# Performance work log

Measured on AMD Instinct MI355X. Metric: run time of the kernel, lower is better.

## Reference

```python
import jax
import jax.numpy as jnp
import numpy as np

ALPHA = 0.95
NUM_POS_FREQS = 4
CROSS_WEIGHT = 0.5
TOPK = 16
EPS = 1e-12


def _pos_enc(coords):
    # coords: [N, 4] -> [N, 4 * 2 * NUM_POS_FREQS]
    N = coords.shape[0]
    freqs = 2.0 ** jnp.arange(NUM_POS_FREQS, dtype=coords.dtype)  # [F]
    angles = coords[:, :, None] * (2.0 * jnp.pi) * freqs          # [N,4,F]
    pe = jnp.concatenate([jnp.sin(angles), jnp.cos(angles)], axis=-1)  # [N,4,2F]
    return pe.reshape(N, -1)


def _cosine_sim(x, y):
    # row-wise cosine similarity: [N,C] x [M,C] -> [N,M]
    xn = x / jnp.maximum(jnp.linalg.norm(x, axis=-1, keepdims=True), EPS)
    yn = y / jnp.maximum(jnp.linalg.norm(y, axis=-1, keepdims=True), EPS)
    return xn @ yn.T


def _sparsify_topk(A, k):
    # row-wise top-k, self-loop always kept (diag forced to max before top-k)
    N = A.shape[0]
    diag = jnp.arange(N)
    A_with_self = A.at[diag, diag].set(jnp.finfo(A.dtype).max)
    _, topk_idx = jax.lax.top_k(A_with_self, k)                   # [N,k]
    mask = jnp.zeros(A.shape, dtype=bool).at[diag[:, None], topk_idx].set(True)
    return jnp.where(mask, A, jnp.zeros((), A.dtype))


def _sym_normalize(A):
    deg = jnp.clip(A.sum(axis=-1, keepdims=True), EPS, None)      # [N,1]
    d_inv_sqrt = deg ** -0.5
    return d_inv_sqrt * A * d_inv_sqrt.T


def _build_adjacency(features, coordinates, history_features, history_coords):
    B, C = features.shape
    n, K, _ = history_features.shape
    H = n * K

    cur_feats = features
    cur_pos = _pos_enc(coordinates)
    A_cur = ALPHA * _cosine_sim(cur_feats, cur_feats) + (1.0 - ALPHA) * _cosine_sim(cur_pos, cur_pos)

    hist_feats = history_features.reshape(H, C)
    hist_pos = _pos_enc(history_coords.reshape(H, 4))
    A_hist = ALPHA * _cosine_sim(hist_feats, hist_feats) + (1.0 - ALPHA) * _cosine_sim(hist_pos, hist_pos)

    A_cross = ALPHA * _cosine_sim(cur_feats, hist_feats) + (1.0 - ALPHA) * _cosine_sim(cur_pos, hist_pos)
    A_cross = CROSS_WEIGHT * A_cross

    A = jnp.block([[A_cur, A_cross], [A_cross.T, A_hist]])        # [N,N], N=B+H
    node_feats = jnp.concatenate([cur_feats, hist_feats], axis=0)

    N = A.shape[0]
    if TOPK is not None and TOPK < N:
        A = _sparsify_topk(A, TOPK)
    A = _sym_normalize(A)
    return A[None], node_feats[None]


def setup_inputs() -> dict:
    key = jax.random.key(0)
    k1, k2, k3, k4 = jax.random.split(key, 4)
    B, C, n, K = 4096, 256, 128, 32
    return {
        "features": jax.random.normal(k1, (B, C), dtype=jnp.float32),
        "coordinates": jax.random.uniform(k2, (B, 4), dtype=jnp.float32),
        "history_features": jax.random.normal(k3, (n, K, C), dtype=jnp.float32),
        "history_coords": jax.random.uniform(k4, (n, K, 4), dtype=jnp.float32),
    }


def reference(features, coordinates, history_features, history_coords):
    adj, node_feats = _build_adjacency(features, coordinates, history_features, history_coords)
    return adj, node_feats
```

## Files before the change

kernel.cpp:

```cpp
#include <hip/hip_runtime.h>
#include <math.h>

#define B_CUR 4096
#define N_TOT 8192
#define C_F   256
#define C_TOT 288
#define KSEL  16
#define NTILE 64

typedef unsigned short u16;
typedef __attribute__((ext_vector_type(8))) short short8;
typedef __attribute__((ext_vector_type(4))) float floatx4;

__device__ inline float bf2f(u16 v) {
  union { unsigned int u; float f; } x; x.u = ((unsigned int)v) << 16; return x.f;
}
__device__ inline u16 f2bf(float f) {
  union { float f; unsigned int u; } x; x.f = f;
  unsigned int u = x.u;
  u += ((u >> 16) & 1u) + 0x7FFFu;
  return (u16)(u >> 16);
}

#define GLD_LDS16(g, l) __builtin_amdgcn_global_load_lds(                      \
    (const __attribute__((address_space(1))) unsigned int*)(g),                \
    (__attribute__((address_space(3))) unsigned int*)(l), 16, 0, 0)

__global__ __launch_bounds__(256) void k_prep(
    const float* __restrict__ feats, const float* __restrict__ hfeats,
    const float* __restrict__ coords, const float* __restrict__ hcoords,
    u16* __restrict__ Zb, float* __restrict__ out_nf) {
  int wave = threadIdx.x >> 6;
  int lane = threadIdx.x & 63;
  int row  = blockIdx.x * 4 + wave;
  const float* src = (row < B_CUR) ? (feats + (size_t)row * C_F)
                                   : (hfeats + (size_t)(row - B_CUR) * C_F);
  int c0 = lane * 4;
  float4 raw = *(const float4*)(src + c0);
  float ss = raw.x*raw.x + raw.y*raw.y + raw.z*raw.z + raw.w*raw.w;
  #pragma unroll
  for (int m = 32; m; m >>= 1) ss += __shfl_xor(ss, m, 64);
  float scale = 0.97467943448089633f / fmaxf(sqrtf(ss), 1e-12f);
  ushort4 o;
  o.x = f2bf(raw.x*scale); o.y = f2bf(raw.y*scale);
  o.z = f2bf(raw.z*scale); o.w = f2bf(raw.w*scale);
  *(ushort4*)(Zb + (size_t)row * C_TOT + c0) = o;
  *(float4*)(out_nf + (size_t)row * C_F + c0) = raw;

  const float* csrc = (row < B_CUR) ? (coords + (size_t)row * 4)
                                    : (hcoords + (size_t)(row - B_CUR) * 4);
  int d = lane >> 3, sc = (lane >> 2) & 1, f = lane & 3;
  float c = csrc[d & 3];
  float ang = c * 6.283185307179586f * (float)(1 << f);
  float pe = sc ? cosf(ang) : sinf(ang);
  float p2 = pe * pe;
  #pragma unroll
  for (int m = 16; m; m >>= 1) p2 += __shfl_xor(p2, m, 64);
  float pscale = 0.22360679774997896f / fmaxf(sqrtf(p2), 1e-12f);
  if (lane < 32) Zb[(size_t)row * C_TOT + C_F + lane] = f2bf(pe * pscale);
}

#define EP_STRIDE 136
__global__ __launch_bounds__(256) void k_gemm_mfma(const u16* __restrict__ Zb,
                                                   u16* __restrict__ adj16) {
  __shared__ __align__(16) u16 smem[2 * 128 * 96];
  u16* As = smem;
  u16* Bs = smem + 128 * 96;
  int tid  = threadIdx.x;

  int t = blockIdx.x;
  int bi = (int)floorf(((2.0f*NTILE + 1.0f) -
            sqrtf((float)((2*NTILE+1)*(2*NTILE+1)) - 8.0f*(float)t)) * 0.5f);
  if (bi < 0) bi = 0; if (bi > NTILE-1) bi = NTILE-1;
  while (bi > 0 && t < bi*NTILE - bi*(bi-1)/2) --bi;
  while (bi < NTILE-1 && t >= (bi+1)*NTILE - (bi+1)*bi/2) ++bi;
  int bj = bi + (t - (bi*NTILE - bi*(bi-1)/2));

  int wave = tid >> 6, lane = tid & 63;
  int quad = lane >> 4, l16 = lane & 15;
  int m0w  = (wave >> 1) * 64;
  int n0w  = (wave & 1) * 64;
  int i0   = bi * 128, j0 = bj * 128;

  floatx4 acc[4][4];
  #pragma unroll
  for (int a = 0; a < 4; ++a)
    #pragma unroll
    for (int b = 0; b < 4; ++b) acc[a][b] = (floatx4){0.f, 0.f, 0.f, 0.f};

  for (int kt = 0; kt < C_TOT; kt += 96) {
    #pragma unroll
    for (int it = 0; it < 6; ++it) {
      int s   = it * 256 + tid;
      int row = s / 12, seg = s % 12;
      const u16* ga = Zb + (size_t)(i0 + row) * C_TOT + kt + seg * 8;
      const u16* gb = Zb + (size_t)(j0 + row) * C_TOT + kt + seg * 8;
      GLD_LDS16(ga, As + s * 8);
      GLD_LDS16(gb, Bs + s * 8);
    }
    __builtin_amdgcn_s_waitcnt(0);
    __syncthreads();
    #pragma unroll
    for (int ks = 0; ks < 3; ++ks) {
      short8 af[4], bf[4];
      #pragma unroll
      for (int mi = 0; mi < 4; ++mi)
        af[mi] = *(const short8*)(&As[(m0w + mi*16 + l16) * 96 + ks*32 + quad*8]);
      #pragma unroll
      for (int ni = 0; ni < 4; ++ni)
        bf[ni] = *(const short8*)(&Bs[(n0w + ni*16 + l16) * 96 + ks*32 + quad*8]);
      #pragma unroll
      for (int mi = 0; mi < 4; ++mi)
        #pragma unroll
        for (int ni = 0; ni < 4; ++ni)
          acc[mi][ni] = __builtin_amdgcn_mfma_f32_16x16x32_bf16(
              af[mi], bf[ni], acc[mi][ni], 0, 0, 0);
    }
    __syncthreads();
  }

  float w = ((bi < 32) != (bj < 32)) ? 0.5f : 1.0f;

  #pragma unroll
  for (int mi = 0; mi < 4; ++mi) {
    #pragma unroll
    for (int ni = 0; ni < 4; ++ni) {
      int col = n0w + ni * 16 + l16;
      #pragma unroll
      for (int rg = 0; rg < 4; ++rg) {
        int row = m0w + mi * 16 + quad * 4 + rg;
        smem[row * EP_STRIDE + col] = f2bf(acc[mi][ni][rg] * w);
      }
    }
  }
  __syncthreads();
  #pragma unroll
  for (int it = 0; it < 8; ++it) {
    int idx = it * 256 + tid;
    int row = idx >> 4, l = idx & 15;
    uint4 v = *(const uint4*)(&smem[row * EP_STRIDE + l * 8]);
    *(uint4*)(&adj16[(size_t)(i0 + row) * 16384 + j0 + l * 8]) = v;
  }

  if (bi != bj) {
    __syncthreads();
    #pragma unroll
    for (int mi = 0; mi < 4; ++mi) {
      #pragma unroll
      for (int ni = 0; ni < 4; ++ni) {
        int col = n0w + ni * 16 + l16;
        #pragma unroll
        for (int rg = 0; rg < 4; ++rg) {
          int row = m0w + mi * 16 + quad * 4 + rg;
          smem[col * EP_STRIDE + row] = f2bf(acc[mi][ni][rg] * w);
        }
      }
    }
    __syncthreads();
    #pragma unroll
    for (int it = 0; it < 8; ++it) {
      int idx = it * 256 + tid;
      int row = idx >> 4, l = idx & 15;
      uint4 v = *(const uint4*)(&smem[row * EP_STRIDE + l * 8]);
      *(uint4*)(&adj16[(size_t)(j0 + row) * 16384 + i0 + l * 8]) = v;
    }
  }
}

__global__ __launch_bounds__(256) void k_topk(
    const u16* adj16, float* adj,
    int* __restrict__ topk_idx, float* __restrict__ topk_val,
    float* __restrict__ deg_out) {
  __shared__ unsigned int cand[64];
  __shared__ float s_diag;
  int r = blockIdx.x;
  int t = threadIdx.x;
  int wave = t >> 6, lane = t & 63;
  const u16* rowp = adj16 + (size_t)r * 16384;

  uint4 raw[4];
  #pragma unroll
  for (int j = 0; j < 4; ++j)
    raw[j] = *(const uint4*)(rowp + j * 2048 + t * 8);
  if (t == 0) s_diag = bf2f(rowp[r]);
  __syncthreads();

  {
    float* oro = adj + (size_t)r * N_TOT;
    const float4 z4 = make_float4(0.f, 0.f, 0.f, 0.f);
    #pragma unroll
    for (int kk = 0; kk < 8; ++kk)
      *(float4*)(oro + kk * 1024 + t * 4) = z4;
  }

  unsigned int keys[32];
  #pragma unroll
  for (int j = 0; j < 4; ++j) {
    int c0 = j * 2048 + t * 8;
    u16 e[8]; *(uint4*)e = raw[j];
    #pragma unroll
    for (int q = 0; q < 8; ++q) {
      int col = c0 + q;
      unsigned int b = e[q];
      unsigned int s16 = (b & 0x8000u) ? (b ^ 0xFFFFu) : (b | 0x8000u);
      unsigned int k = (s16 << 16) | (unsigned int)(8191 - col);
      if (col == r) k = 0xFFFF0000u | (unsigned int)(8191 - r);
      keys[j * 8 + q] = k;
    }
  }

  unsigned int m1 = 0, m2 = 0; int i1 = 0, i2 = 0;
  #pragma unroll
  for (int i = 0; i < 32; ++i) {
    unsigned int k = keys[i];
    if (k > m1) { m2 = m1; i2 = i1; m1 = k; i1 = i; }
    else if (k > m2) { m2 = k; i2 = i; }
  }
  unsigned int taken = 0;

  for (int it = 0; it < KSEL; ++it) {
    unsigned int wmax = m1;
    #pragma unroll
    for (int s = 32; s; s >>= 1) {
      unsigned int o = (unsigned int)__shfl_xor((int)wmax, s, 64);
      wmax = (o > wmax) ? o : wmax;
    }
    if (lane == it) cand[wave * 16 + it] = wmax;
    if (m1 == wmax && m1 != 0) {
      taken |= 1u << i1;
      if (m2 != 0) { m1 = m2; i1 = i2; m2 = 0; }
      else {
        m1 = 0; m2 = 0; i1 = 0; i2 = 0;
        #pragma unroll
        for (int i = 0; i < 32; ++i) {
          unsigned int k = (taken & (1u << i)) ? 0u : keys[i];
          if (k > m1) { m2 = m1; i2 = i1; m1 = k; i1 = i; }
          else if (k > m2) { m2 = k; i2 = i; }
        }
      }
    }
  }
  __syncthreads();

  if (wave == 0) {
    unsigned int c = cand[lane];
    unsigned int myWin = 0;
    for (int it = 0; it < KSEL; ++it) {
      unsigned int wmax = c;
      #pragma unroll
      for (int s = 32; s; s >>= 1) {
        unsigned int o = (unsigned int)__shfl_xor((int)wmax, s, 64);
        wmax = (o > wmax) ? o : wmax;
      }
      if (c == wmax) c = 0;
      if (lane == it) myWin = wmax;
    }
    float val = 0.f;
    int col = 0;
    if (lane < KSEL) {
      unsigned int p = myWin;
      col = 8191 - (int)(p & 0x1FFFu);
      unsigned int k16 = p >> 16;
      unsigned int b = (k16 & 0x8000u) ? (k16 ^ 0x8000u) : ((~k16) & 0xFFFFu);
      val = (col == r) ? s_diag : bf2f((u16)b);
      topk_idx[r * KSEL + lane] = col;
      topk_val[r * KSEL + lane] = val;
    }
    float s = (lane < KSEL) ? val : 0.f;
    #pragma unroll
    for (int m = 8; m; m >>= 1) s += __shfl_xor(s, m, 64);
    if (lane == 0) deg_out[r] = s;
  }
}

__global__ void k_scale(float* __restrict__ adj, const int* __restrict__ topk_idx,
                        const float* __restrict__ topk_val,
                        const float* __restrict__ deg) {
  int g = blockIdx.x * blockDim.x + threadIdx.x;
  if (g >= N_TOT * KSEL) return;
  int r = g >> 4, m = g & 15;
  int j = topk_idx[r * KSEL + m];
  if (j < 0) j = 0; if (j >= N_TOT) j = N_TOT - 1;
  float v = topk_val[r * KSEL + m];
  float di = 1.0f / sqrtf(fmaxf(deg[r], 1e-12f));
  float dj = 1.0f / sqrtf(fmaxf(deg[j], 1e-12f));
  adj[(size_t)r * N_TOT + j] = v * di * dj;
}

extern "C" void kernel_launch(void* const* d_in, const int* in_sizes, int n_in,
                              void* d_out, int out_size, void* d_ws, size_t ws_size,
                              hipStream_t stream) {
  const float* feats   = (const float*)d_in[0];
  const float* coords  = (const float*)d_in[1];
  const float* hfeats  = (const float*)d_in[2];
  const float* hcoords = (const float*)d_in[3];
  float* out    = (float*)d_out;
  float* adj    = out;
  u16*   adj16  = (u16*)out;
  float* out_nf = out + (size_t)N_TOT * N_TOT;

  char* ws    = (char*)d_ws;
  u16*  Zb    = (u16*)ws;
  size_t zb   = (size_t)N_TOT * C_TOT * sizeof(u16);
  zb = (zb + 255) & ~(size_t)255;
  int*   t_idx = (int*)(ws + zb);
  float* t_val = (float*)(ws + zb + (size_t)N_TOT*KSEL*sizeof(int));
  float* deg   = (float*)(ws + zb + (size_t)N_TOT*KSEL*(sizeof(int)+sizeof(float)));

  hipLaunchKernelGGL(k_prep, dim3(N_TOT/4), dim3(256), 0, stream,
                     feats, hfeats, coords, hcoords, Zb, out_nf);
  hipLaunchKernelGGL(k_gemm_mfma, dim3(NTILE*(NTILE+1)/2), dim3(256), 0, stream,
                     Zb, adj16);
  hipLaunchKernelGGL(k_topk, dim3(N_TOT), dim3(256), 0, stream,
                     adj16, adj, t_idx, t_val, deg);
  hipLaunchKernelGGL(k_scale, dim3((N_TOT*KSEL + 255)/256), dim3(256), 0, stream,
                     adj, t_idx, t_val, deg);
}
```

Baseline: 386.7 us.

## Double-buffer GEMM K-loop, move bf16 scores to workspace, nontemporal zero stores

The GEMM K-loop now uses 32-wide K slices with double-buffered LDS, so the next slice's global-to-LDS loads overlap the MFMAs on the current one. The bf16 score matrix moves out of the output buffer, where it was stored with a 16384 stride, into a separate workspace region with a compact 8192 stride. That lets k_topk drop a barrier and zero its output rows with nontemporal stores without clobbering unread scores. The cost is more loop iterations and barriers in the GEMM, plus extra workspace memory.

```diff
diff --git a/kernel.cpp b/kernel.cpp
--- a/kernel.cpp
+++ b/kernel.cpp
@@ -62,10 +62,8 @@
 
 #define EP_STRIDE 136
 __global__ __launch_bounds__(256) void k_gemm_mfma(const u16* __restrict__ Zb,
-                                                   u16* __restrict__ adj16) {
-  __shared__ __align__(16) u16 smem[2 * 128 * 96];
-  u16* As = smem;
-  u16* Bs = smem + 128 * 96;
+                                                   u16* __restrict__ s16) {
+  __shared__ __align__(16) u16 smem[17408];
   int tid  = threadIdx.x;
 
   int t = blockIdx.x;
@@ -82,40 +80,59 @@
   int n0w  = (wave & 1) * 64;
   int i0   = bi * 128, j0 = bj * 128;
 
+  int srow0 = tid >> 2;
+  int scol0 = (tid & 3) * 8;
+
   floatx4 acc[4][4];
   #pragma unroll
   for (int a = 0; a < 4; ++a)
     #pragma unroll
     for (int b = 0; b < 4; ++b) acc[a][b] = (floatx4){0.f, 0.f, 0.f, 0.f};
 
-  for (int kt = 0; kt < C_TOT; kt += 96) {
-    #pragma unroll
-    for (int it = 0; it < 6; ++it) {
-      int s   = it * 256 + tid;
-      int row = s / 12, seg = s % 12;
-      const u16* ga = Zb + (size_t)(i0 + row) * C_TOT + kt + seg * 8;
-      const u16* gb = Zb + (size_t)(j0 + row) * C_TOT + kt + seg * 8;
-      GLD_LDS16(ga, As + s * 8);
-      GLD_LDS16(gb, Bs + s * 8);
-    }
-    __builtin_amdgcn_s_waitcnt(0);
-    __syncthreads();
-    #pragma unroll
-    for (int ks = 0; ks < 3; ++ks) {
-      short8 af[4], bf[4];
-      #pragma unroll
-      for (int mi = 0; mi < 4; ++mi)
-        af[mi] = *(const short8*)(&As[(m0w + mi*16 + l16) * 96 + ks*32 + quad*8]);
+  {
+    const u16* ga0 = Zb + (size_t)(i0 + srow0) * C_TOT + scol0;
+    const u16* gb0 = Zb + (size_t)(j0 + srow0) * C_TOT + scol0;
+    const u16* ga1 = Zb + (size_t)(i0 + srow0 + 64) * C_TOT + scol0;
+    const u16* gb1 = Zb + (size_t)(j0 + srow0 + 64) * C_TOT + scol0;
+    GLD_LDS16(ga0, smem + 0    + tid * 8);
+    GLD_LDS16(ga1, smem + 0    + (tid + 256) * 8);
+    GLD_LDS16(gb0, smem + 4096 + tid * 8);
+    GLD_LDS16(gb1, smem + 4096 + (tid + 256) * 8);
+  }
+  __builtin_amdgcn_s_waitcnt(0);
+  __syncthreads();
+
+  for (int i = 0; i < 9; ++i) {
+    int p = i & 1;
+    if (i < 8) {
+      int kt = (i + 1) * 32;
+      u16* dstA = smem + (p ^ 1) * 8192;
+      u16* dstB = dstA + 4096;
+      const u16* ga0 = Zb + (size_t)(i0 + srow0) * C_TOT + kt + scol0;
+      const u16* gb0 = Zb + (size_t)(j0 + srow0) * C_TOT + kt + scol0;
+      const u16* ga1 = Zb + (size_t)(i0 + srow0 + 64) * C_TOT + kt + scol0;
+      const u16* gb1 = Zb + (size_t)(j0 + srow0 + 64) * C_TOT + kt + scol0;
+      GLD_LDS16(ga0, dstA + tid * 8);
+      GLD_LDS16(ga1, dstA + (tid + 256) * 8);
+      GLD_LDS16(gb0, dstB + tid * 8);
+      GLD_LDS16(gb1, dstB + (tid + 256) * 8);
+    }
+    const u16* As = smem + p * 8192;
+    const u16* Bs = As + 4096;
+    short8 af[4], bf[4];
+    #pragma unroll
+    for (int mi = 0; mi < 4; ++mi)
+      af[mi] = *(const short8*)(&As[(m0w + mi*16 + l16) * 32 + quad * 8]);
+    #pragma unroll
+    for (int ni = 0; ni < 4; ++ni)
+      bf[ni] = *(const short8*)(&Bs[(n0w + ni*16 + l16) * 32 + quad * 8]);
+    #pragma unroll
+    for (int mi = 0; mi < 4; ++mi)
       #pragma unroll
       for (int ni = 0; ni < 4; ++ni)
-        bf[ni] = *(const short8*)(&Bs[(n0w + ni*16 + l16) * 96 + ks*32 + quad*8]);
-      #pragma unroll
-      for (int mi = 0; mi < 4; ++mi)
-        #pragma unroll
-        for (int ni = 0; ni < 4; ++ni)
-          acc[mi][ni] = __builtin_amdgcn_mfma_f32_16x16x32_bf16(
-              af[mi], bf[ni], acc[mi][ni], 0, 0, 0);
-    }
+        acc[mi][ni] = __builtin_amdgcn_mfma_f32_16x16x32_bf16(
+            af[mi], bf[ni], acc[mi][ni], 0, 0, 0);
+    __builtin_amdgcn_s_waitcnt(0);
     __syncthreads();
   }
 
@@ -139,7 +156,7 @@
     int idx = it * 256 + tid;
     int row = idx >> 4, l = idx & 15;
     uint4 v = *(const uint4*)(&smem[row * EP_STRIDE + l * 8]);
-    *(uint4*)(&adj16[(size_t)(i0 + row) * 16384 + j0 + l * 8]) = v;
+    *(uint4*)(&s16[(size_t)(i0 + row) * N_TOT + j0 + l * 8]) = v;
   }
 
   if (bi != bj) {
@@ -162,13 +179,13 @@
       int idx = it * 256 + tid;
       int row = idx >> 4, l = idx & 15;
       uint4 v = *(const uint4*)(&smem[row * EP_STRIDE + l * 8]);
-      *(uint4*)(&adj16[(size_t)(j0 + row) * 16384 + i0 + l * 8]) = v;
+      *(uint4*)(&s16[(size_t)(j0 + row) * N_TOT + i0 + l * 8]) = v;
     }
   }
 }
 
 __global__ __launch_bounds__(256) void k_topk(
-    const u16* adj16, float* adj,
+    const u16* __restrict__ s16, float* __restrict__ adj,
     int* __restrict__ topk_idx, float* __restrict__ topk_val,
     float* __restrict__ deg_out) {
   __shared__ unsigned int cand[64];
@@ -176,21 +193,20 @@
   int r = blockIdx.x;
   int t = threadIdx.x;
   int wave = t >> 6, lane = t & 63;
-  const u16* rowp = adj16 + (size_t)r * 16384;
+  const u16* rowp = s16 + (size_t)r * N_TOT;
 
   uint4 raw[4];
   #pragma unroll
   for (int j = 0; j < 4; ++j)
     raw[j] = *(const uint4*)(rowp + j * 2048 + t * 8);
   if (t == 0) s_diag = bf2f(rowp[r]);
-  __syncthreads();
 
   {
     float* oro = adj + (size_t)r * N_TOT;
-    const float4 z4 = make_float4(0.f, 0.f, 0.f, 0.f);
+    const floatx4 z4 = (floatx4){0.f, 0.f, 0.f, 0.f};
     #pragma unroll
     for (int kk = 0; kk < 8; ++kk)
-      *(float4*)(oro + kk * 1024 + t * 4) = z4;
+      __builtin_nontemporal_store(z4, (floatx4*)(oro + kk * 1024 + t * 4));
   }
 
   unsigned int keys[32];
@@ -202,8 +218,8 @@
     for (int q = 0; q < 8; ++q) {
       int col = c0 + q;
       unsigned int b = e[q];
-      unsigned int s16 = (b & 0x8000u) ? (b ^ 0xFFFFu) : (b | 0x8000u);
-      unsigned int k = (s16 << 16) | (unsigned int)(8191 - col);
+      unsigned int s16v = (b & 0x8000u) ? (b ^ 0xFFFFu) : (b | 0x8000u);
+      unsigned int k = (s16v << 16) | (unsigned int)(8191 - col);
       if (col == r) k = 0xFFFF0000u | (unsigned int)(8191 - r);
       keys[j * 8 + q] = k;
     }
@@ -296,7 +312,6 @@
   const float* hcoords = (const float*)d_in[3];
   float* out    = (float*)d_out;
   float* adj    = out;
-  u16*   adj16  = (u16*)out;
   float* out_nf = out + (size_t)N_TOT * N_TOT;
 
   char* ws    = (char*)d_ws;
@@ -306,13 +321,14 @@
   int*   t_idx = (int*)(ws + zb);
   float* t_val = (float*)(ws + zb + (size_t)N_TOT*KSEL*sizeof(int));
   float* deg   = (float*)(ws + zb + (size_t)N_TOT*KSEL*(sizeof(int)+sizeof(float)));
+  u16*   s16   = (u16*)(ws + (16u << 20));
 
   hipLaunchKernelGGL(k_prep, dim3(N_TOT/4), dim3(256), 0, stream,
                      feats, hfeats, coords, hcoords, Zb, out_nf);
   hipLaunchKernelGGL(k_gemm_mfma, dim3(NTILE*(NTILE+1)/2), dim3(256), 0, stream,
-                     Zb, adj16);
+                     Zb, s16);
   hipLaunchKernelGGL(k_topk, dim3(N_TOT), dim3(256), 0, stream,
-                     adj16, adj, t_idx, t_val, deg);
+                     s16, adj, t_idx, t_val, deg);
   hipLaunchKernelGGL(k_scale, dim3((N_TOT*KSEL + 255)/256), dim3(256), 0, stream,
                      adj, t_idx, t_val, deg);
 }
```

After: 394.7 us. 2.1% more time.
